# Performance work log

Hardware: AMD Instinct MI355X
Metric: run time of the kernel (lower is better)

The kernel has to match this reference:

```python
import jax, jax.numpy as jnp
import numpy as np

S, B, D, H, HD = 2048, 1, 1280, 16, 80
NSEQ = 8  # packed sequences

def setup_inputs() -> dict:
    key = jax.random.key(0)
    k1, k2, k3 = jax.random.split(key, 3)
    x = jax.random.normal(k1, (S, B, D), dtype=jnp.float32)
    # cu_seqlens: 8 equal packed segments, starts at 0, ends at S
    cu_seqlens = (jnp.arange(NSEQ + 1, dtype=jnp.int32) * (S // NSEQ))
    W_qkv = jax.random.normal(k2, (3 * D, D), dtype=jnp.float32) * (1.0 / np.sqrt(D))
    b_qkv = jax.random.normal(k3, (3 * D,), dtype=jnp.float32) * 0.01
    return {"x": x, "cu_seqlens": cu_seqlens, "W_qkv": W_qkv, "b_qkv": b_qkv}

def _block_diag_mask(cu_seqlens, s):
    # segment id of each position; positions in the same segment attend to each other
    pos = jnp.arange(s)
    seg = jnp.searchsorted(cu_seqlens[1:], pos, side='right')  # [s]
    return seg[:, None] == seg[None, :]  # [s, s] bool

def reference(x, cu_seqlens, W_qkv, b_qkv):
    s, b, d = x.shape
    qkv = jnp.einsum('sbd,ed->sbe', x, W_qkv) + b_qkv  # [s,b,3d]
    q, k, v = jnp.split(qkv, 3, axis=2)
    # [s,b,h,hd] -> [b,h,s,hd]
    def to_bhsd(t):
        return t.reshape(s, b, H, HD).transpose(1, 2, 0, 3)
    q1, k1, v1 = to_bhsd(q), to_bhsd(k), to_bhsd(v)
    mask = _block_diag_mask(cu_seqlens, s)  # [s,s]
    scale = 1.0 / np.sqrt(HD)
    scores = jnp.einsum('bhsd,bhtd->bhst', q1, k1) * scale  # [b,h,s,s]
    neg = jnp.finfo(scores.dtype).min
    scores = jnp.where(mask[None, None, :, :], scores, neg)
    attn = jax.nn.softmax(scores, axis=-1)
    out = jnp.einsum('bhst,bhtd->bhsd', attn, v1)  # [b,h,s,hd]
    return out.transpose(0, 2, 1, 3)  # [b,s,h,hd]
```

## Files before the change

kernel.cpp:

```cpp
#include <hip/hip_runtime.h>
#include <hip/hip_bf16.h>

#define S_LEN 2048
#define DIM 1280
#define NH 16
#define HD 80
#define NE 3840
#define SEG 256
#define NSEG 8
#define QKV_SZ (NH * S_LEN * HD)
#define NX (S_LEN * DIM)
#define NW (NE * DIM)

typedef short short8 __attribute__((ext_vector_type(8)));
typedef float floatx4 __attribute__((ext_vector_type(4)));

__device__ inline unsigned short f2bf(float f) {
    unsigned int u = __float_as_uint(f);
    return (unsigned short)((u + 0x7fffu + ((u >> 16) & 1u)) >> 16);
}

__global__ __launch_bounds__(256) void convert_bf16_kernel(
    const float* __restrict__ x, const float* __restrict__ W,
    unsigned short* __restrict__ xb, unsigned short* __restrict__ Wb)
{
    const int gi = blockIdx.x * 256 + threadIdx.x;
    const float* src;
    unsigned short* dst;
    int off;
    if (gi < NX / 4) { src = x; dst = xb; off = gi * 4; }
    else             { src = W; dst = Wb; off = (gi - NX / 4) * 4; }
    float4 v = *(const float4*)(src + off);
    ushort4 o;
    o.x = f2bf(v.x); o.y = f2bf(v.y); o.z = f2bf(v.z); o.w = f2bf(v.w);
    *(ushort4*)(dst + off) = o;
}

__global__ __launch_bounds__(256) void qkv_gemm_kernel(
    const unsigned short* __restrict__ xb,
    const unsigned short* __restrict__ Wb,
    const float* __restrict__ bias,
    unsigned short* __restrict__ qkvb)
{
    __shared__ short As[128 * 32];
    __shared__ short Bs[128 * 32];
    __shared__ short Vt[128 * 72];

    const int tid  = threadIdx.x;
    const int w    = tid >> 6;
    const int lane = tid & 63;
    const int m0 = blockIdx.y * 128;
    const int n0 = blockIdx.x * 128;

    const int rsub = lane >> 2;
    const int ksub = lane & 3;
    const int ar0 = 32 * w + rsub;
    const int ar1 = 32 * w + 16 + rsub;
    const unsigned short* agp0 = xb + (size_t)(m0 + ar0) * DIM + ksub * 8;
    const unsigned short* agp1 = xb + (size_t)(m0 + ar1) * DIM + ksub * 8;
    const unsigned short* bgp0 = Wb + (size_t)(n0 + ar0) * DIM + ksub * 8;
    const unsigned short* bgp1 = Wb + (size_t)(n0 + ar1) * DIM + ksub * 8;
    short* alp0 = &As[ar0 * 32 + ksub * 8];
    short* alp1 = &As[ar1 * 32 + ksub * 8];
    short* blp0 = &Bs[ar0 * 32 + ksub * 8];
    short* blp1 = &Bs[ar1 * 32 + ksub * 8];

    const int warow = (w >> 1) * 64;
    const int wacol = (w & 1) * 64;
    const int quad = lane >> 4;
    const int lm   = lane & 15;

    floatx4 acc[4][4];
    #pragma unroll
    for (int i = 0; i < 4; ++i)
        #pragma unroll
        for (int j = 0; j < 4; ++j)
            acc[i][j] = (floatx4){0.f, 0.f, 0.f, 0.f};

    for (int k0 = 0; k0 < DIM; k0 += 32) {
        __syncthreads();
        __builtin_amdgcn_global_load_lds(
            (const __attribute__((address_space(1))) unsigned int*)(agp0 + k0),
            (__attribute__((address_space(3))) unsigned int*)alp0, 16, 0, 0);
        __builtin_amdgcn_global_load_lds(
            (const __attribute__((address_space(1))) unsigned int*)(agp1 + k0),
            (__attribute__((address_space(3))) unsigned int*)alp1, 16, 0, 0);
        __builtin_amdgcn_global_load_lds(
            (const __attribute__((address_space(1))) unsigned int*)(bgp0 + k0),
            (__attribute__((address_space(3))) unsigned int*)blp0, 16, 0, 0);
        __builtin_amdgcn_global_load_lds(
            (const __attribute__((address_space(1))) unsigned int*)(bgp1 + k0),
            (__attribute__((address_space(3))) unsigned int*)blp1, 16, 0, 0);
        __syncthreads();

        short8 a[4], b[4];
        #pragma unroll
        for (int i = 0; i < 4; ++i)
            a[i] = *(const short8*)&As[(warow + i * 16 + lm) * 32 + quad * 8];
        #pragma unroll
        for (int j = 0; j < 4; ++j)
            b[j] = *(const short8*)&Bs[(wacol + j * 16 + lm) * 32 + quad * 8];
        #pragma unroll
        for (int i = 0; i < 4; ++i)
            #pragma unroll
            for (int j = 0; j < 4; ++j)
                acc[i][j] = __builtin_amdgcn_mfma_f32_16x16x32_bf16(
                    a[i], b[j], acc[i][j], 0, 0, 0);
    }

    const int which = n0 / DIM;
    const int nrem0 = n0 - which * DIM;

    if (which < 2) {
        #pragma unroll
        for (int j = 0; j < 4; ++j) {
            const int nrem = nrem0 + wacol + j * 16 + lm;
            const float bv = bias[which * DIM + nrem];
            const int hh = nrem / HD;
            const int hd = nrem - hh * HD;
            unsigned short* hp = qkvb + (size_t)which * QKV_SZ
                               + (size_t)hh * (S_LEN * HD) + hd;
            #pragma unroll
            for (int i = 0; i < 4; ++i) {
                const int mbase = m0 + warow + i * 16 + quad * 4;
                #pragma unroll
                for (int r = 0; r < 4; ++r)
                    hp[(size_t)(mbase + r) * HD] = f2bf(acc[i][j][r] + bv);
            }
        }
    } else {
        unsigned short* Vg = qkvb + 2 * (size_t)QKV_SZ;
        #pragma unroll
        for (int hh2 = 0; hh2 < 2; ++hh2) {
            __syncthreads();
            if ((w >> 1) == hh2) {
                #pragma unroll
                for (int j = 0; j < 4; ++j) {
                    const int nn = wacol + j * 16 + lm;
                    const float bv = bias[2 * DIM + nrem0 + nn];
                    #pragma unroll
                    for (int i = 0; i < 4; ++i) {
                        const int mloc = i * 16 + quad * 4;
                        #pragma unroll
                        for (int t = 0; t < 2; ++t) {
                            const unsigned pk =
                                ((unsigned)f2bf(acc[i][j][2 * t + 1] + bv) << 16)
                              | (unsigned)f2bf(acc[i][j][2 * t] + bv);
                            *(unsigned*)&Vt[nn * 72 + mloc + 2 * t] = pk;
                        }
                    }
                }
            }
            __syncthreads();
            #pragma unroll
            for (int rnd = 0; rnd < 4; ++rnd) {
                const int nn = rnd * 32 + (tid >> 3);
                const int ml = (tid & 7) * 8;
                const int nrem = nrem0 + nn;
                const int hhh = nrem / HD;
                const int hd = nrem - hhh * HD;
                unsigned short* gp = Vg + (size_t)hhh * (HD * S_LEN)
                                   + (size_t)hd * S_LEN + m0 + 64 * hh2 + ml;
                *(short8*)gp = *(const short8*)&Vt[nn * 72 + ml];
            }
        }
    }
}

__global__ __launch_bounds__(256) void attn_kernel(
    const unsigned short* __restrict__ Qb,
    const unsigned short* __restrict__ Kb,
    const unsigned short* __restrict__ Vb,
    float* __restrict__ out)
{
    __shared__ short KVs[128 * 104];
    __shared__ short Ps[64 * 136];
    __shared__ float rsl[4][64];

    const int qc  = blockIdx.x;
    const int h   = blockIdx.y;
    const int seg = blockIdx.z;
    const int tid = threadIdx.x;
    const int w    = tid >> 6;
    const int lane = tid & 63;
    const int quad = lane >> 4;
    const int lm   = lane & 15;
    const int qbase = seg * SEG + qc * 64;
    const float scale = 0.11180339887498948f;
    const short8 zfrag = {0, 0, 0, 0, 0, 0, 0, 0};

    short8 aQ[4][3];
    #pragma unroll
    for (int mt = 0; mt < 4; ++mt) {
        const unsigned short* qp = Qb + ((size_t)h * S_LEN + qbase + mt * 16 + lm) * HD;
        #pragma unroll
        for (int ks = 0; ks < 3; ++ks) {
            const int hd0 = ks * 32 + quad * 8;
            aQ[mt][ks] = (hd0 < 80) ? *(const short8*)(qp + hd0) : zfrag;
        }
    }

    floatx4 Oacc[5];
    #pragma unroll
    for (int nt = 0; nt < 5; ++nt) Oacc[nt] = (floatx4){0.f, 0.f, 0.f, 0.f};
    float rsp[4][4];
    #pragma unroll
    for (int mt = 0; mt < 4; ++mt)
        #pragma unroll
        for (int r = 0; r < 4; ++r) rsp[mt][r] = 0.0f;

    for (int half = 0; half < 2; ++half) {
        const int k0g = seg * SEG + half * 128;

        __syncthreads();
        {
            const unsigned short* src = Kb + ((size_t)h * S_LEN + k0g) * HD;
            #pragma unroll
            for (int rnd = 0; rnd < 5; ++rnd) {
                const int f = rnd * 256 + tid;
                const int key = f / 10;
                const int c = f - key * 10;
                *(short8*)&KVs[key * 104 + c * 8] = *(const short8*)(src + key * 80 + c * 8);
            }
            const int zkey = tid >> 1;
            const int zc = tid & 1;
            *(short8*)&KVs[zkey * 104 + 80 + zc * 8] = zfrag;
        }
        __syncthreads();

        floatx4 Cs[4][2];
        #pragma unroll
        for (int mt = 0; mt < 4; ++mt)
            #pragma unroll
            for (int nt = 0; nt < 2; ++nt) Cs[mt][nt] = (floatx4){0.f, 0.f, 0.f, 0.f};

        #pragma unroll
        for (int ks = 0; ks < 3; ++ks) {
            short8 b[2];
            #pragma unroll
            for (int nt = 0; nt < 2; ++nt)
                b[nt] = *(const short8*)&KVs[(w * 32 + nt * 16 + lm) * 104 + ks * 32 + quad * 8];
            #pragma unroll
            for (int mt = 0; mt < 4; ++mt)
                #pragma unroll
                for (int nt = 0; nt < 2; ++nt)
                    Cs[mt][nt] = __builtin_amdgcn_mfma_f32_16x16x32_bf16(
                        aQ[mt][ks], b[nt], Cs[mt][nt], 0, 0, 0);
        }

        #pragma unroll
        for (int mt = 0; mt < 4; ++mt)
            #pragma unroll
            for (int nt = 0; nt < 2; ++nt)
                #pragma unroll
                for (int r = 0; r < 4; ++r) {
                    const float p = __expf(Cs[mt][nt][r] * scale);
                    rsp[mt][r] += p;
                    const float po = __shfl_xor(p, 1);
                    if ((lm & 1) == 0) {
                        const unsigned pk = ((unsigned)f2bf(po) << 16) | (unsigned)f2bf(p);
                        *(unsigned*)&Ps[(mt * 16 + quad * 4 + r) * 136 + w * 32 + nt * 16 + lm] = pk;
                    }
                }
        __syncthreads();

        {
            const unsigned short* src = Vb + (size_t)h * (HD * S_LEN) + k0g;
            #pragma unroll
            for (int rnd = 0; rnd < 5; ++rnd) {
                const int f = rnd * 256 + tid;
                const int hd = f >> 4;
                const int sc = f & 15;
                *(short8*)&KVs[hd * 136 + sc * 8] = *(const short8*)(src + hd * S_LEN + sc * 8);
            }
        }
        __syncthreads();

        #pragma unroll
        for (int ks2 = 0; ks2 < 4; ++ks2) {
            const short8 a = *(const short8*)&Ps[(w * 16 + lm) * 136 + ks2 * 32 + quad * 8];
            #pragma unroll
            for (int nt = 0; nt < 5; ++nt) {
                const short8 b = *(const short8*)&KVs[(nt * 16 + lm) * 136 + ks2 * 32 + quad * 8];
                Oacc[nt] = __builtin_amdgcn_mfma_f32_16x16x32_bf16(a, b, Oacc[nt], 0, 0, 0);
            }
        }
    }

    #pragma unroll
    for (int mt = 0; mt < 4; ++mt)
        #pragma unroll
        for (int r = 0; r < 4; ++r) {
            float v = rsp[mt][r];
            v += __shfl_xor(v, 1);
            v += __shfl_xor(v, 2);
            v += __shfl_xor(v, 4);
            v += __shfl_xor(v, 8);
            if (lm == 0) rsl[w][mt * 16 + quad * 4 + r] = v;
        }
    __syncthreads();

    #pragma unroll
    for (int r = 0; r < 4; ++r) {
        const int row = w * 16 + quad * 4 + r;
        const float l = rsl[0][row] + rsl[1][row] + rsl[2][row] + rsl[3][row];
        const float linv = 1.0f / l;
        float* op = out + (size_t)(qbase + row) * (NH * HD) + h * HD;
        #pragma unroll
        for (int nt = 0; nt < 5; ++nt)
            op[nt * 16 + lm] = Oacc[nt][r] * linv;
    }
}

extern "C" void kernel_launch(void* const* d_in, const int* in_sizes, int n_in,
                              void* d_out, int out_size, void* d_ws, size_t ws_size,
                              hipStream_t stream)
{
    const float* x      = (const float*)d_in[0];
    const float* W_qkv  = (const float*)d_in[2];
    const float* b_qkv  = (const float*)d_in[3];
    float* out = (float*)d_out;

    unsigned short* xb = (unsigned short*)d_ws;
    unsigned short* Wb = xb + NX;
    unsigned short* qkvb = Wb + NW;
    unsigned short* Qb = qkvb;
    unsigned short* Kb = qkvb + QKV_SZ;
    unsigned short* Vb = qkvb + 2 * (size_t)QKV_SZ;

    convert_bf16_kernel<<<(NX + NW) / 4 / 256, 256, 0, stream>>>(x, W_qkv, xb, Wb);
    qkv_gemm_kernel<<<dim3(NE / 128, S_LEN / 128), 256, 0, stream>>>(xb, Wb, b_qkv, qkvb);
    attn_kernel<<<dim3(4, NH, NSEG), 256, 0, stream>>>(Qb, Kb, Vb, out);
}
```

Before: 130.7 us.

## Double GEMM k-tile to 64 and halve attention query tile per block

The QKV GEMM now loads a 64-wide k slice per iteration, four rows per thread, which halves the number of barrier-synchronised load phases while doubling LDS use for the A/B tiles. The attention kernel processes 32 query rows per block instead of 64 and doubles the grid. PV output tiles are split across warps by m-tile and by 3/2 column groups. This raises block count and occupancy for attention. The cost is that K and V are reloaded from global memory twice as often, and the PV work is unevenly split across warps.

```diff
diff --git a/kernel.cpp b/kernel.cpp
--- a/kernel.cpp
+++ b/kernel.cpp
@@ -42,8 +42,8 @@
     const float* __restrict__ bias,
     unsigned short* __restrict__ qkvb)
 {
-    __shared__ short As[128 * 32];
-    __shared__ short Bs[128 * 32];
+    __shared__ short As[128 * 64];
+    __shared__ short Bs[128 * 64];
     __shared__ short Vt[128 * 72];
 
     const int tid  = threadIdx.x;
@@ -52,18 +52,20 @@
     const int m0 = blockIdx.y * 128;
     const int n0 = blockIdx.x * 128;
 
-    const int rsub = lane >> 2;
-    const int ksub = lane & 3;
-    const int ar0 = 32 * w + rsub;
-    const int ar1 = 32 * w + 16 + rsub;
-    const unsigned short* agp0 = xb + (size_t)(m0 + ar0) * DIM + ksub * 8;
-    const unsigned short* agp1 = xb + (size_t)(m0 + ar1) * DIM + ksub * 8;
-    const unsigned short* bgp0 = Wb + (size_t)(n0 + ar0) * DIM + ksub * 8;
-    const unsigned short* bgp1 = Wb + (size_t)(n0 + ar1) * DIM + ksub * 8;
-    short* alp0 = &As[ar0 * 32 + ksub * 8];
-    short* alp1 = &As[ar1 * 32 + ksub * 8];
-    short* blp0 = &Bs[ar0 * 32 + ksub * 8];
-    short* blp1 = &Bs[ar1 * 32 + ksub * 8];
+    const int row8 = lane >> 3;
+    const int k8   = (lane & 7) * 8;
+    const unsigned short* agp[4];
+    const unsigned short* bgp[4];
+    short* alp[4];
+    short* blp[4];
+    #pragma unroll
+    for (int c = 0; c < 4; ++c) {
+        const int r = w * 32 + c * 8 + row8;
+        agp[c] = xb + (size_t)(m0 + r) * DIM + k8;
+        bgp[c] = Wb + (size_t)(n0 + r) * DIM + k8;
+        alp[c] = &As[r * 64 + k8];
+        blp[c] = &Bs[r * 64 + k8];
+    }
 
     const int warow = (w >> 1) * 64;
     const int wacol = (w & 1) * 64;
@@ -77,35 +79,35 @@
         for (int j = 0; j < 4; ++j)
             acc[i][j] = (floatx4){0.f, 0.f, 0.f, 0.f};
 
-    for (int k0 = 0; k0 < DIM; k0 += 32) {
-        __syncthreads();
-        __builtin_amdgcn_global_load_lds(
-            (const __attribute__((address_space(1))) unsigned int*)(agp0 + k0),
-            (__attribute__((address_space(3))) unsigned int*)alp0, 16, 0, 0);
-        __builtin_amdgcn_global_load_lds(
-            (const __attribute__((address_space(1))) unsigned int*)(agp1 + k0),
-            (__attribute__((address_space(3))) unsigned int*)alp1, 16, 0, 0);
-        __builtin_amdgcn_global_load_lds(
-            (const __attribute__((address_space(1))) unsigned int*)(bgp0 + k0),
-            (__attribute__((address_space(3))) unsigned int*)blp0, 16, 0, 0);
-        __builtin_amdgcn_global_load_lds(
-            (const __attribute__((address_space(1))) unsigned int*)(bgp1 + k0),
-            (__attribute__((address_space(3))) unsigned int*)blp1, 16, 0, 0);
-        __syncthreads();
-
-        short8 a[4], b[4];
-        #pragma unroll
-        for (int i = 0; i < 4; ++i)
-            a[i] = *(const short8*)&As[(warow + i * 16 + lm) * 32 + quad * 8];
-        #pragma unroll
-        for (int j = 0; j < 4; ++j)
-            b[j] = *(const short8*)&Bs[(wacol + j * 16 + lm) * 32 + quad * 8];
-        #pragma unroll
-        for (int i = 0; i < 4; ++i)
+    for (int k0 = 0; k0 < DIM; k0 += 64) {
+        __syncthreads();
+        #pragma unroll
+        for (int c = 0; c < 4; ++c) {
+            __builtin_amdgcn_global_load_lds(
+                (const __attribute__((address_space(1))) unsigned int*)(agp[c] + k0),
+                (__attribute__((address_space(3))) unsigned int*)alp[c], 16, 0, 0);
+            __builtin_amdgcn_global_load_lds(
+                (const __attribute__((address_space(1))) unsigned int*)(bgp[c] + k0),
+                (__attribute__((address_space(3))) unsigned int*)blp[c], 16, 0, 0);
+        }
+        __syncthreads();
+
+        #pragma unroll
+        for (int ks = 0; ks < 2; ++ks) {
+            short8 a[4], b[4];
+            #pragma unroll
+            for (int i = 0; i < 4; ++i)
+                a[i] = *(const short8*)&As[(warow + i * 16 + lm) * 64 + ks * 32 + quad * 8];
             #pragma unroll
             for (int j = 0; j < 4; ++j)
-                acc[i][j] = __builtin_amdgcn_mfma_f32_16x16x32_bf16(
-                    a[i], b[j], acc[i][j], 0, 0, 0);
+                b[j] = *(const short8*)&Bs[(wacol + j * 16 + lm) * 64 + ks * 32 + quad * 8];
+            #pragma unroll
+            for (int i = 0; i < 4; ++i)
+                #pragma unroll
+                for (int j = 0; j < 4; ++j)
+                    acc[i][j] = __builtin_amdgcn_mfma_f32_16x16x32_bf16(
+                        a[i], b[j], acc[i][j], 0, 0, 0);
+        }
     }
 
     const int which = n0 / DIM;
@@ -174,8 +176,8 @@
     float* __restrict__ out)
 {
     __shared__ short KVs[128 * 104];
-    __shared__ short Ps[64 * 136];
-    __shared__ float rsl[4][64];
+    __shared__ short Ps[32 * 136];
+    __shared__ float rsl[4][32];
 
     const int qc  = blockIdx.x;
     const int h   = blockIdx.y;
@@ -185,13 +187,13 @@
     const int lane = tid & 63;
     const int quad = lane >> 4;
     const int lm   = lane & 15;
-    const int qbase = seg * SEG + qc * 64;
+    const int qbase = seg * SEG + qc * 32;
     const float scale = 0.11180339887498948f;
     const short8 zfrag = {0, 0, 0, 0, 0, 0, 0, 0};
 
-    short8 aQ[4][3];
-    #pragma unroll
-    for (int mt = 0; mt < 4; ++mt) {
+    short8 aQ[2][3];
+    #pragma unroll
+    for (int mt = 0; mt < 2; ++mt) {
         const unsigned short* qp = Qb + ((size_t)h * S_LEN + qbase + mt * 16 + lm) * HD;
         #pragma unroll
         for (int ks = 0; ks < 3; ++ks) {
@@ -200,12 +202,16 @@
         }
     }
 
-    floatx4 Oacc[5];
-    #pragma unroll
-    for (int nt = 0; nt < 5; ++nt) Oacc[nt] = (floatx4){0.f, 0.f, 0.f, 0.f};
-    float rsp[4][4];
-    #pragma unroll
-    for (int mt = 0; mt < 4; ++mt)
+    const int mtile  = w >> 1;
+    const int ntbase = (w & 1) ? 3 : 0;
+    const int ntcnt  = (w & 1) ? 2 : 3;
+
+    floatx4 Oacc[3];
+    #pragma unroll
+    for (int t = 0; t < 3; ++t) Oacc[t] = (floatx4){0.f, 0.f, 0.f, 0.f};
+    float rsp[2][4];
+    #pragma unroll
+    for (int mt = 0; mt < 2; ++mt)
         #pragma unroll
         for (int r = 0; r < 4; ++r) rsp[mt][r] = 0.0f;
 
@@ -228,9 +234,9 @@
         }
         __syncthreads();
 
-        floatx4 Cs[4][2];
-        #pragma unroll
-        for (int mt = 0; mt < 4; ++mt)
+        floatx4 Cs[2][2];
+        #pragma unroll
+        for (int mt = 0; mt < 2; ++mt)
             #pragma unroll
             for (int nt = 0; nt < 2; ++nt) Cs[mt][nt] = (floatx4){0.f, 0.f, 0.f, 0.f};
 
@@ -241,7 +247,7 @@
             for (int nt = 0; nt < 2; ++nt)
                 b[nt] = *(const short8*)&KVs[(w * 32 + nt * 16 + lm) * 104 + ks * 32 + quad * 8];
             #pragma unroll
-            for (int mt = 0; mt < 4; ++mt)
+            for (int mt = 0; mt < 2; ++mt)
                 #pragma unroll
                 for (int nt = 0; nt < 2; ++nt)
                     Cs[mt][nt] = __builtin_amdgcn_mfma_f32_16x16x32_bf16(
@@ -249,7 +255,7 @@
         }
 
         #pragma unroll
-        for (int mt = 0; mt < 4; ++mt)
+        for (int mt = 0; mt < 2; ++mt)
             #pragma unroll
             for (int nt = 0; nt < 2; ++nt)
                 #pragma unroll
@@ -278,17 +284,20 @@
 
         #pragma unroll
         for (int ks2 = 0; ks2 < 4; ++ks2) {
-            const short8 a = *(const short8*)&Ps[(w * 16 + lm) * 136 + ks2 * 32 + quad * 8];
-            #pragma unroll
-            for (int nt = 0; nt < 5; ++nt) {
-                const short8 b = *(const short8*)&KVs[(nt * 16 + lm) * 136 + ks2 * 32 + quad * 8];
-                Oacc[nt] = __builtin_amdgcn_mfma_f32_16x16x32_bf16(a, b, Oacc[nt], 0, 0, 0);
-            }
-        }
-    }
-
-    #pragma unroll
-    for (int mt = 0; mt < 4; ++mt)
+            const short8 a = *(const short8*)&Ps[(mtile * 16 + lm) * 136 + ks2 * 32 + quad * 8];
+            #pragma unroll
+            for (int t = 0; t < 3; ++t) {
+                if (t < ntcnt) {
+                    const int nt = ntbase + t;
+                    const short8 b = *(const short8*)&KVs[(nt * 16 + lm) * 136 + ks2 * 32 + quad * 8];
+                    Oacc[t] = __builtin_amdgcn_mfma_f32_16x16x32_bf16(a, b, Oacc[t], 0, 0, 0);
+                }
+            }
+        }
+    }
+
+    #pragma unroll
+    for (int mt = 0; mt < 2; ++mt)
         #pragma unroll
         for (int r = 0; r < 4; ++r) {
             float v = rsp[mt][r];
@@ -302,13 +311,14 @@
 
     #pragma unroll
     for (int r = 0; r < 4; ++r) {
-        const int row = w * 16 + quad * 4 + r;
+        const int row = mtile * 16 + quad * 4 + r;
         const float l = rsl[0][row] + rsl[1][row] + rsl[2][row] + rsl[3][row];
         const float linv = 1.0f / l;
         float* op = out + (size_t)(qbase + row) * (NH * HD) + h * HD;
         #pragma unroll
-        for (int nt = 0; nt < 5; ++nt)
-            op[nt * 16 + lm] = Oacc[nt][r] * linv;
+        for (int t = 0; t < 3; ++t)
+            if (t < ntcnt)
+                op[(ntbase + t) * 16 + lm] = Oacc[t][r] * linv;
     }
 }
 
@@ -330,5 +340,5 @@
 
     convert_bf16_kernel<<<(NX + NW) / 4 / 256, 256, 0, stream>>>(x, W_qkv, xb, Wb);
     qkv_gemm_kernel<<<dim3(NE / 128, S_LEN / 128), 256, 0, stream>>>(xb, Wb, b_qkv, qkvb);
-    attn_kernel<<<dim3(4, NH, NSEG), 256, 0, stream>>>(Qb, Kb, Vb, out);
-}
+    attn_kernel<<<dim3(8, NH, NSEG), 256, 0, stream>>>(Qb, Kb, Vb, out);
+}
```

New measurement: 159.5 us. +22.0%, slower.
